# Kernel tuning notes

Measured on AMD Instinct MI355X. Metric: run time of the kernel, lower is better.

The kernel has to match this reference:

```python
import jax, jax.numpy as jnp
import numpy as np

B, C, N, K, C_OUT = 16, 64, 2048, 3, 64


def setup_inputs() -> dict:
    key = jax.random.key(0)
    k1, k2, k3 = jax.random.split(key, 3)
    x = jax.random.normal(k1, (B, C, N), dtype=jnp.float32)
    # Conv1d params: weight [out_ch, in_ch, K], bias [out_ch]
    fan_in = C * K
    bound = 1.0 / np.sqrt(fan_in)
    W = jax.random.uniform(k2, (C_OUT, C, K), dtype=jnp.float32, minval=-bound, maxval=bound)
    b = jax.random.uniform(k3, (C_OUT,), dtype=jnp.float32, minval=-bound, maxval=bound)
    return {"x": x, "W": W, "b": b}


def reference(x, W, b):
    # x: [B, C, N]
    # pairwise squared-distance matrix over the length dim: [B, N, N]
    norm_sq = jnp.sum(x * x, axis=1, keepdims=True)              # [B, 1, N]
    dot = jnp.einsum('bcn,bcm->bnm', x, x)                       # [B, N, N]
    dist = norm_sq + jnp.swapaxes(norm_sq, 1, 2) - 2.0 * dot     # [B, N, N]
    # K smallest distances per point (self included, dist=0)
    _, idx = jax.lax.top_k(-dist, K)                             # [B, N, K]
    # gather neighbors: prime[b, c, n*K + k] = x[b, c, idx[b, n, k]]
    idx_flat = idx.reshape(B, 1, N * K)
    prime = jnp.take_along_axis(x, jnp.broadcast_to(idx_flat, (B, C, N * K)), axis=2)
    # Conv1d(kernel=K, stride=K, padding=0) -> [B, C_OUT, N]
    out = jax.lax.conv_general_dilated(
        prime, W, window_strides=(K,), padding='VALID',
        dimension_numbers=('NCH', 'OIH', 'NCH'))
    out = out + b[None, :, None]
    return jax.nn.relu(out)
```

## Files before the change

### kernel.cpp

```cpp
#include <hip/hip_runtime.h>
#include <float.h>

#define BB 16
#define CC 64
#define NN 2048
#define KNN 3
#define COUT 64
#define SPL 8
#define TILES 8

typedef _Float16 half8 __attribute__((ext_vector_type(8)));
typedef float f32x16 __attribute__((ext_vector_type(16)));

union u4h8 { uint4 v; half8 h; };

__device__ __forceinline__ void gl_lds16(const void* g, void* l) {
    __builtin_amdgcn_global_load_lds(
        (const __attribute__((address_space(1))) unsigned*)g,
        (__attribute__((address_space(3))) unsigned*)l, 16, 0, 0);
}

__global__ __launch_bounds__(256) void k_prep(const float* __restrict__ x,
                                              uint4* __restrict__ xe,
                                              unsigned* __restrict__ anc) {
    __shared__ float t[64][65];
    __shared__ float nsh[64];
    const int b = blockIdx.x;
    const int n0 = blockIdx.y * 64;
    const int tid = threadIdx.x;
    const int ln = tid & 63, g = tid >> 6;
#pragma unroll
    for (int i = 0; i < 16; ++i) {
        const int c = g + 4 * i;
        t[c][ln] = x[((size_t)b * CC + c) * NN + n0 + ln];
    }
    __syncthreads();
    if (tid < 64) {
        float s = 0.f;
#pragma unroll
        for (int c = 0; c < 64; ++c) s = fmaf(t[c][tid], t[c][tid], s);
        nsh[tid] = s;
    }
#pragma unroll
    for (int i = 0; i < 4; ++i) {
        const int cid = tid + 256 * i;
        const int lane = cid & 63;
        const int kblk = (cid >> 6) & 7;
        const int ctl = cid >> 9;
        const int m = ctl * 32 + (lane & 31);
        const int khalf = (lane >> 5) * 8;
        union { uint4 v; _Float16 h[8]; } pk;
#pragma unroll
        for (int j = 0; j < 8; ++j) {
            const int kg = kblk * 16 + khalf + j;
            const int ch = kg & 63;
            const float f = t[ch][m];
            const _Float16 hi = (_Float16)f;
            pk.h[j] = (kg < 64) ? hi : (_Float16)(f - (float)hi);
        }
        const int ct = (n0 >> 5) + ctl;
        xe[((size_t)(b * 64 + ct) * 8 + kblk) * 64 + lane] = pk.v;
    }
    __syncthreads();
    if (tid < 64) {
        const int ctl = tid >> 5, l = tid & 31;
        const int ct = (n0 >> 5) + ctl;
        const float h = -0.5f * nsh[ctl * 32 + l];
        const _Float16 a0 = (_Float16)h;
        const _Float16 a1 = (_Float16)(h - (float)a0);
        union { unsigned u; _Float16 hh[2]; } cu;
        cu.hh[0] = a0; cu.hh[1] = a1;
        anc[(size_t)(b * 64 + ct) * 32 + l] = cu.u;
    }
}

__global__ __launch_bounds__(256) void k_wprep(const float* __restrict__ W,
                                               uint4* __restrict__ Wf) {
    const int tid = threadIdx.x;
#pragma unroll
    for (int i = 0; i < 6; ++i) {
        const int id = tid + 256 * i;
        const int l = id & 63;
        const int kb = (id >> 6) & 3;
        const int ct2 = (id >> 8) & 1;
        const int kk = id >> 9;
        const int co = ct2 * 32 + (l & 31);
        union { uint4 v; _Float16 h[8]; } pk;
#pragma unroll
        for (int j = 0; j < 8; ++j) {
            const int c = kb * 16 + 8 * (l >> 5) + j;
            pk.h[j] = (_Float16)W[(co * CC + c) * KNN + kk];
        }
        Wf[id] = pk.v;
    }
}

__global__ __launch_bounds__(512, 4) void k_top3(const uint4* __restrict__ xe,
                                                 const unsigned* __restrict__ anc,
                                                 uint4* __restrict__ pk) {
    __shared__ uint4 buf[4096];
    const int bid = blockIdx.x;
    const int qb = bid >> 7;
    const int rem = bid & 127;
    const int b = rem >> 3;
    const int s = rem & 7;

    const int tid = threadIdx.x;
    const int lane = tid & 63;
    const int w = tid >> 6;
    const int qg = qb * 8 + w;

    const uint4* xb = xe + (size_t)(b * 64) * 512;
    const int ct0 = s * TILES;
    const uint4* gsrc = xb + (size_t)ct0 * 512;

#pragma unroll
    for (int i = 0; i < 8; ++i) {
        const int c = w * 8 + i;
        gl_lds16(gsrc + (size_t)c * 64 + lane, &buf[c * 64]);
    }

    half8 bq[8];
#pragma unroll
    for (int kb = 0; kb < 8; ++kb) {
        u4h8 tq;
        tq.v = xe[((size_t)(b * 64 + qg) * 8 + kb) * 64 + lane];
        bq[kb] = tq.h;
    }
    unsigned av_u[TILES];
#pragma unroll
    for (int t = 0; t < TILES; ++t)
        av_u[t] = anc[(size_t)(b * 64 + ct0 + t) * 32 + (lane & 31)];

    half8 bnc = {};
    if (lane < 32) { bnc[0] = (_Float16)1.0f; bnc[1] = (_Float16)1.0f; }

    float k0 = -FLT_MAX, k1 = -FLT_MAX, k2 = -FLT_MAX;
    int i0 = 0, i1 = 0, i2 = 0;
    const int hi4 = (lane >> 5) * 4;

    __syncthreads();

#pragma unroll
    for (int t = 0; t < TILES; ++t) {
        f32x16 acc = {};
        {
            u4h8 ah[4];
#pragma unroll
            for (int kb = 0; kb < 4; ++kb) ah[kb].v = buf[(t * 8 + kb) * 64 + lane];
#pragma unroll
            for (int kb = 0; kb < 4; ++kb)
                acc = __builtin_amdgcn_mfma_f32_32x32x16_f16(ah[kb].h, bq[kb], acc, 0, 0, 0);
#pragma unroll
            for (int kb = 0; kb < 4; ++kb)
                acc = __builtin_amdgcn_mfma_f32_32x32x16_f16(ah[kb].h, bq[kb + 4], acc, 0, 0, 0);
        }
        {
            u4h8 al[4];
#pragma unroll
            for (int kb = 0; kb < 4; ++kb) al[kb].v = buf[(t * 8 + 4 + kb) * 64 + lane];
#pragma unroll
            for (int kb = 0; kb < 4; ++kb)
                acc = __builtin_amdgcn_mfma_f32_32x32x16_f16(al[kb].h, bq[kb], acc, 0, 0, 0);
            half8 av = {};
            union { unsigned u; _Float16 hh[2]; } cu;
            cu.u = av_u[t];
            av[0] = cu.hh[0]; av[1] = cu.hh[1];
            acc = __builtin_amdgcn_mfma_f32_32x32x16_f16(av, bnc, acc, 0, 0, 0);
        }

        const int libase = t * 32 + hi4;
#pragma unroll
        for (int j = 0; j < 16; ++j) {
            const float a = acc[j];
            const int li = libase + (j & 3) + 8 * (j >> 2);
            const bool g0 = a > k0;
            const float d0 = g0 ? k0 : a;  const int di0 = g0 ? i0 : li;
            k0 = g0 ? a : k0;              i0 = g0 ? li : i0;
            const bool g1 = d0 > k1;
            const float d1 = g1 ? k1 : d0; const int di1 = g1 ? i1 : di0;
            k1 = g1 ? d0 : k1;             i1 = g1 ? di0 : i1;
            const bool g2 = d1 > k2;
            k2 = g2 ? d1 : k2;             i2 = g2 ? di1 : i2;
        }
    }

    const float ok0 = __shfl_xor(k0, 32), ok1 = __shfl_xor(k1, 32), ok2 = __shfl_xor(k2, 32);
    const int oi0 = __shfl_xor(i0, 32), oi1 = __shfl_xor(i1, 32), oi2 = __shfl_xor(i2, 32);
    const float oks[3] = {ok0, ok1, ok2};
    const int ois[3] = {oi0, oi1, oi2};
#pragma unroll
    for (int r = 0; r < 3; ++r) {
        const float c = oks[r]; const int ci = ois[r];
        const bool g0 = (c > k0) || (c == k0 && ci < i0);
        const float d0 = g0 ? k0 : c;  const int di0 = g0 ? i0 : ci;
        k0 = g0 ? c : k0;              i0 = g0 ? ci : i0;
        const bool g1 = (d0 > k1) || (d0 == k1 && di0 < i1);
        const float d1 = g1 ? k1 : d0; const int di1 = g1 ? i1 : di0;
        k1 = g1 ? d0 : k1;             i1 = g1 ? di0 : i1;
        const bool g2 = (d1 > k2) || (d1 == k2 && di1 < i2);
        k2 = g2 ? d1 : k2;             i2 = g2 ? di1 : i2;
    }
    if (lane < 32) {
        const int q = qg * 32 + lane;
        uint4 v;
        v.x = __float_as_uint(k0);
        v.y = __float_as_uint(k1);
        v.z = __float_as_uint(k2);
        v.w = (unsigned)i0 | ((unsigned)i1 << 8) | ((unsigned)i2 << 16);
        pk[((size_t)b * SPL + s) * NN + q] = v;
    }
}

__global__ __launch_bounds__(256) void k_merge(const uint4* __restrict__ pk,
                                               int* __restrict__ fi) {
    const int t = blockIdx.x * 256 + threadIdx.x;
    if (t >= BB * NN) return;
    const int b = t / NN, n = t % NN;
    float dv[3 * SPL]; int iv[3 * SPL];
#pragma unroll
    for (int s = 0; s < SPL; ++s) {
        const uint4 v = pk[((size_t)b * SPL + s) * NN + n];
        dv[s * 3 + 0] = __uint_as_float(v.x);
        dv[s * 3 + 1] = __uint_as_float(v.y);
        dv[s * 3 + 2] = __uint_as_float(v.z);
        iv[s * 3 + 0] = (int)(v.w & 255u) + s * 256;
        iv[s * 3 + 1] = (int)((v.w >> 8) & 255u) + s * 256;
        iv[s * 3 + 2] = (int)((v.w >> 16) & 255u) + s * 256;
    }
    float bd = FLT_MAX; int bi = -1;
#pragma unroll
    for (int r = 0; r < 3; ++r) {
        float ck = -FLT_MAX; int ci = 0x7fffffff;
#pragma unroll
        for (int j = 0; j < 3 * SPL; ++j) {
            const bool after_prev = (dv[j] < bd) || (dv[j] == bd && iv[j] > bi);
            const bool better = (dv[j] > ck) || (dv[j] == ck && iv[j] < ci);
            if (after_prev && better) { ck = dv[j]; ci = iv[j]; }
        }
        fi[(size_t)t * 3 + r] = ci;
        bd = ck; bi = ci;
    }
}

__global__ __launch_bounds__(256) void k_conv(const uint4* __restrict__ xe,
                                              const uint4* __restrict__ Wf,
                                              const int* __restrict__ fi,
                                              const float* __restrict__ bias,
                                              float* __restrict__ out) {
    __shared__ float ot[64][65];
    const int b = blockIdx.y;
    const int n0 = blockIdx.x * 64;
    const int tid = threadIdx.x;
    const int l = tid & 63;
    const int w = tid >> 6;
    const int mt = w >> 1, ct2 = w & 1;
    const int p31 = l & 31, kh = l >> 5;
    const int npt = n0 + mt * 32 + p31;

    f32x16 acc = {};
    const uint4* xb = xe + (size_t)b * 64 * 8 * 64;
    const int fbase3 = (b * NN + npt) * KNN;
#pragma unroll
    for (int kk = 0; kk < KNN; ++kk) {
        const int src = fi[fbase3 + kk];
        const uint4* ap = xb + (size_t)(src >> 5) * 512 + (src & 31) + 32 * kh;
        uint4 af[4], bw[4];
#pragma unroll
        for (int kb = 0; kb < 4; ++kb) af[kb] = ap[(size_t)kb * 64];
#pragma unroll
        for (int kb = 0; kb < 4; ++kb) bw[kb] = Wf[((kk * 2 + ct2) * 4 + kb) * 64 + l];
#pragma unroll
        for (int kb = 0; kb < 4; ++kb) {
            u4h8 ua, ub;
            ua.v = af[kb]; ub.v = bw[kb];
            acc = __builtin_amdgcn_mfma_f32_32x32x16_f16(ua.h, ub.h, acc, 0, 0, 0);
        }
    }
    const int co = ct2 * 32 + p31;
    const float bv = bias[co];
#pragma unroll
    for (int j = 0; j < 16; ++j) {
        const int pt = mt * 32 + (j & 3) + 8 * (j >> 2) + 4 * kh;
        ot[co][pt] = fmaxf(acc[j] + bv, 0.f);
    }
    __syncthreads();
#pragma unroll
    for (int i = 0; i < 16; ++i) {
        const int v = tid + 256 * i;
        const int co2 = v >> 6, col = v & 63;
        out[((size_t)(b * COUT + co2)) * NN + n0 + col] = ot[co2][col];
    }
}

extern "C" void kernel_launch(void* const* d_in, const int* in_sizes, int n_in,
                              void* d_out, int out_size, void* d_ws, size_t ws_size,
                              hipStream_t stream) {
    const float* x = (const float*)d_in[0];
    const float* W = (const float*)d_in[1];
    const float* bias = (const float*)d_in[2];
    float* out = (float*)d_out;

    char* ws = (char*)d_ws;
    uint4* xe = (uint4*)(ws);
    unsigned* anc = (unsigned*)(ws + 8388608);
    uint4* Wf = (uint4*)(ws + 8519680);
    uint4* pk = (uint4*)(ws + 8544256);
    int* fi = (int*)(ws + 12738560);

    k_prep<<<dim3(BB, NN / 64), 256, 0, stream>>>(x, xe, anc);
    k_wprep<<<1, 256, 0, stream>>>(W, Wf);
    k_top3<<<dim3(8 * 128), 512, 0, stream>>>(xe, anc, pk);
    k_merge<<<(BB * NN + 255) / 256, 256, 0, stream>>>(pk, fi);
    k_conv<<<dim3(NN / 64, BB), 256, 0, stream>>>(xe, Wf, fi, bias, out);
}
```

Baseline: 74.74 us.

## Use value-only med3 top-3 pass then recompute tiles to recover indices

Replaces the per-element compare/select insertion network, which tracked both values and indices, with a value-only top-3 update using fmax and fmed3. A second pass recomputes every MFMA tile and matches the final values to recover their indices. This cuts VALU work in the selection loop but doubles the MFMA and LDS-read work. It also changes tie-breaking, since the last matching position wins and duplicate values can map to the same index.

```diff
diff --git a/kernel.cpp b/kernel.cpp
--- a/kernel.cpp
+++ b/kernel.cpp
@@ -95,6 +95,29 @@
     }
 }
 
+#define COMPUTE_TILE(T, ACC)                                                      \
+    {                                                                             \
+        u4h8 ah[4];                                                               \
+        _Pragma("unroll")                                                         \
+        for (int kb = 0; kb < 4; ++kb) ah[kb].v = buf[((T) * 8 + kb) * 64 + lane];\
+        _Pragma("unroll")                                                         \
+        for (int kb = 0; kb < 4; ++kb)                                  \
+            ACC = __builtin_amdgcn_mfma_f32_32x32x16_f16(ah[kb].h, bq[kb], ACC, 0, 0, 0); \
+        _Pragma("unroll")                                                         \
+        for (int kb = 0; kb < 4; ++kb)                                  \
+            ACC = __builtin_amdgcn_mfma_f32_32x32x16_f16(ah[kb].h, bq[kb + 4], ACC, 0, 0, 0); \
+        u4h8 al[4];                                                               \
+        _Pragma("unroll")                                                         \
+        for (int kb = 0; kb < 4; ++kb) al[kb].v = buf[((T) * 8 + 4 + kb) * 64 + lane]; \
+        _Pragma("unroll")                                                         \
+        for (int kb = 0; kb < 4; ++kb)                                  \
+            ACC = __builtin_amdgcn_mfma_f32_32x32x16_f16(al[kb].h, bq[kb], ACC, 0, 0, 0); \
+        half8 av = {};                                                            \
+        { union { unsigned u; _Float16 hh[2]; } cu; cu.u = av_u[(T)];             \
+          av[0] = cu.hh[0]; av[1] = cu.hh[1]; }                                   \
+        ACC = __builtin_amdgcn_mfma_f32_32x32x16_f16(av, bnc, ACC, 0, 0, 0);      \
+    }
+
 __global__ __launch_bounds__(512, 4) void k_top3(const uint4* __restrict__ xe,
                                                  const unsigned* __restrict__ anc,
                                                  uint4* __restrict__ pk) {
@@ -136,7 +159,6 @@
     if (lane < 32) { bnc[0] = (_Float16)1.0f; bnc[1] = (_Float16)1.0f; }
 
     float k0 = -FLT_MAX, k1 = -FLT_MAX, k2 = -FLT_MAX;
-    int i0 = 0, i1 = 0, i2 = 0;
     const int hi4 = (lane >> 5) * 4;
 
     __syncthreads();
@@ -144,46 +166,34 @@
 #pragma unroll
     for (int t = 0; t < TILES; ++t) {
         f32x16 acc = {};
-        {
-            u4h8 ah[4];
-#pragma unroll
-            for (int kb = 0; kb < 4; ++kb) ah[kb].v = buf[(t * 8 + kb) * 64 + lane];
-#pragma unroll
-            for (int kb = 0; kb < 4; ++kb)
-                acc = __builtin_amdgcn_mfma_f32_32x32x16_f16(ah[kb].h, bq[kb], acc, 0, 0, 0);
-#pragma unroll
-            for (int kb = 0; kb < 4; ++kb)
-                acc = __builtin_amdgcn_mfma_f32_32x32x16_f16(ah[kb].h, bq[kb + 4], acc, 0, 0, 0);
-        }
-        {
-            u4h8 al[4];
-#pragma unroll
-            for (int kb = 0; kb < 4; ++kb) al[kb].v = buf[(t * 8 + 4 + kb) * 64 + lane];
-#pragma unroll
-            for (int kb = 0; kb < 4; ++kb)
-                acc = __builtin_amdgcn_mfma_f32_32x32x16_f16(al[kb].h, bq[kb], acc, 0, 0, 0);
-            half8 av = {};
-            union { unsigned u; _Float16 hh[2]; } cu;
-            cu.u = av_u[t];
-            av[0] = cu.hh[0]; av[1] = cu.hh[1];
-            acc = __builtin_amdgcn_mfma_f32_32x32x16_f16(av, bnc, acc, 0, 0, 0);
-        }
-
-        const int libase = t * 32 + hi4;
+        COMPUTE_TILE(t, acc)
 #pragma unroll
         for (int j = 0; j < 16; ++j) {
             const float a = acc[j];
-            const int li = libase + (j & 3) + 8 * (j >> 2);
-            const bool g0 = a > k0;
-            const float d0 = g0 ? k0 : a;  const int di0 = g0 ? i0 : li;
-            k0 = g0 ? a : k0;              i0 = g0 ? li : i0;
-            const bool g1 = d0 > k1;
-            const float d1 = g1 ? k1 : d0; const int di1 = g1 ? i1 : di0;
-            k1 = g1 ? d0 : k1;             i1 = g1 ? di0 : i1;
-            const bool g2 = d1 > k2;
-            k2 = g2 ? d1 : k2;             i2 = g2 ? di1 : i2;
-        }
-    }
+            const float n0 = fmaxf(k0, a);
+            const float n1 = __builtin_amdgcn_fmed3f(k0, k1, a);
+            const float n2 = __builtin_amdgcn_fmed3f(k1, k2, a);
+            k0 = n0; k1 = n1; k2 = n2;
+        }
+    }
+
+    int p0 = 0, p1 = 0, p2 = 0;
+#pragma unroll
+    for (int t = 0; t < TILES; ++t) {
+        f32x16 acc = {};
+        COMPUTE_TILE(t, acc)
+#pragma unroll
+        for (int j = 0; j < 16; ++j) {
+            const float a = acc[j];
+            const int m = t * 16 + j;
+            p0 = (a == k0) ? m : p0;
+            p1 = (a == k1) ? m : p1;
+            p2 = (a == k2) ? m : p2;
+        }
+    }
+    int i0 = (p0 >> 4) * 32 + (p0 & 3) + 8 * ((p0 >> 2) & 3) + hi4;
+    int i1 = (p1 >> 4) * 32 + (p1 & 3) + 8 * ((p1 >> 2) & 3) + hi4;
+    int i2 = (p2 >> 4) * 32 + (p2 & 3) + 8 * ((p2 >> 2) & 3) + hi4;
 
     const float ok0 = __shfl_xor(k0, 32), ok1 = __shfl_xor(k1, 32), ok2 = __shfl_xor(k2, 32);
     const int oi0 = __shfl_xor(i0, 32), oi1 = __shfl_xor(i1, 32), oi2 = __shfl_xor(i2, 32);
```

New measurement: 119.6 us. 1.6x slower.
